# Optimization experiments

Measured on AMD Instinct MI355X. Metric: run time of the kernel, lower is better.

The kernel has to match this reference:

```python
import jax, jax.numpy as jnp
import numpy as np

D_MODEL = 1024
NUM_HEADS = 16
D_K = D_MODEL // NUM_HEADS
LOCAL_WINDOW = 3
STRIDE = 4


def strided_mask(seq_len):
    # position i attends to j iff j <= i and (i-j <= local_window or (i-j) % stride == 0)
    i = jnp.arange(seq_len)[:, None]
    j = jnp.arange(seq_len)[None, :]
    d = i - j
    return (d >= 0) & ((d <= LOCAL_WINDOW) | (d % STRIDE == 0))


def setup_inputs() -> dict:
    key = jax.random.key(0)
    ks = jax.random.split(key, 11)
    B, S, D = 4, 1024, D_MODEL
    s = 1.0 / np.sqrt(D)
    inp = {
        "Q": jax.random.normal(ks[0], (B, S, D), jnp.float32),
        "K": jax.random.normal(ks[1], (B, S, D), jnp.float32),
        "V": jax.random.normal(ks[2], (B, S, D), jnp.float32),
        "Wq": jax.random.normal(ks[3], (D, D), jnp.float32) * s,
        "bq": jnp.zeros((D,), jnp.float32),
        "Wk": jax.random.normal(ks[4], (D, D), jnp.float32) * s,
        "bk": jnp.zeros((D,), jnp.float32),
        "Wv": jax.random.normal(ks[5], (D, D), jnp.float32) * s,
        "bv": jnp.zeros((D,), jnp.float32),
        "Wo": jax.random.normal(ks[6], (D, D), jnp.float32) * s,
        "bo": jnp.zeros((D,), jnp.float32),
    }
    return inp


def reference(Q, K, V, Wq, bq, Wk, bk, Wv, bv, Wo, bo):
    B, S, D = Q.shape
    H, dk = NUM_HEADS, D_K

    def split(x):  # [B,S,D] -> [B,H,S,dk]
        return x.reshape(B, S, H, dk).transpose(0, 2, 1, 3)

    q = split(Q @ Wq + bq)
    k = split(K @ Wk + bk)
    v = split(V @ Wv + bv)

    scores = jnp.einsum("bhsd,bhtd->bhst", q, k) / jnp.sqrt(
        jnp.asarray(dk, jnp.float32))
    m = strided_mask(S)[None, None]  # [1,1,S,S]
    scores = jnp.where(m, scores, -1e9)
    attn = jax.nn.softmax(scores, axis=-1)
    out = jnp.einsum("bhst,bhtd->bhsd", attn, v)
    out = out.transpose(0, 2, 1, 3).reshape(B, S, D)  # combine heads
    return out @ Wo + bo
```

## Files before the change

kernel.cpp:

```cpp
#include <hip/hip_runtime.h>

typedef _Float16 f16;
typedef __attribute__((ext_vector_type(8))) _Float16 f16x8;
typedef __attribute__((ext_vector_type(4))) _Float16 f16x4;
typedef __attribute__((ext_vector_type(4))) float f32x4;

#define MFMA16(a, b, c) __builtin_amdgcn_mfma_f32_16x16x32_f16((a), (b), (c), 0, 0, 0)

__device__ __forceinline__ void gld_lds16(const void* g, void* l) {
  __builtin_amdgcn_global_load_lds(
      (__attribute__((address_space(1))) void*)const_cast<void*>(g),
      (__attribute__((address_space(3))) void*)l, 16, 0, 0);
}

__device__ __forceinline__ f16x8 ld8(const f16* p) { return *(const f16x8*)p; }

__global__ __launch_bounds__(256) void cvt_x_kernel(
    const float* __restrict__ Q, const float* __restrict__ K, const float* __restrict__ V,
    f16* __restrict__ oq, f16* __restrict__ ok, f16* __restrict__ ov) {
  const float* src = blockIdx.z == 0 ? Q : (blockIdx.z == 1 ? K : V);
  f16* dst = blockIdx.z == 0 ? oq : (blockIdx.z == 1 ? ok : ov);
  size_t i = ((size_t)blockIdx.x * 256 + threadIdx.x) * 8;
  float4 a = *(const float4*)(src + i);
  float4 b = *(const float4*)(src + i + 4);
  f16x8 h;
  h[0] = (f16)a.x; h[1] = (f16)a.y; h[2] = (f16)a.z; h[3] = (f16)a.w;
  h[4] = (f16)b.x; h[5] = (f16)b.y; h[6] = (f16)b.z; h[7] = (f16)b.w;
  *(f16x8*)(dst + i) = h;
}

__global__ __launch_bounds__(256) void cvt_wT_kernel(
    const float* __restrict__ Wq, const float* __restrict__ Wk,
    const float* __restrict__ Wv, const float* __restrict__ Wo,
    f16* __restrict__ Tq, f16* __restrict__ Tk, f16* __restrict__ Tv, f16* __restrict__ To) {
  const int z = blockIdx.z;
  const float* W = z == 0 ? Wq : (z == 1 ? Wk : (z == 2 ? Wv : Wo));
  f16* T = z == 0 ? Tq : (z == 1 ? Tk : (z == 2 ? Tv : To));
  __shared__ float tile[64][65];
  const int k0 = blockIdx.x * 64, n0 = blockIdx.y * 64;
  const int tx = threadIdx.x & 63, ty = threadIdx.x >> 6;
#pragma unroll
  for (int rr = 0; rr < 16; ++rr) {
    int r = rr * 4 + ty;
    tile[r][tx] = W[(size_t)(k0 + r) * 1024 + n0 + tx];
  }
  __syncthreads();
#pragma unroll
  for (int rr = 0; rr < 16; ++rr) {
    int nn = rr * 4 + ty;
    T[(size_t)(n0 + nn) * 1024 + k0 + tx] = (f16)tile[tx][nn];
  }
}

__global__ __launch_bounds__(256) void gemm_qkv_kernel(
    const f16* __restrict__ Xq, const f16* __restrict__ Xk, const f16* __restrict__ Xv,
    const f16* __restrict__ Bq, const f16* __restrict__ Bk, const f16* __restrict__ Bv,
    const float* __restrict__ bq, const float* __restrict__ bk, const float* __restrict__ bv,
    f16* __restrict__ qh, f16* __restrict__ kg,
    f16* __restrict__ vh, f16* __restrict__ vtg) {
  const int z = blockIdx.z;
  const f16* A = z == 0 ? Xq : (z == 1 ? Xk : Xv);
  const f16* Bt = z == 0 ? Bq : (z == 1 ? Bk : Bv);
  const float* bias = z == 0 ? bq : (z == 1 ? bk : bv);

  __shared__ alignas(16) f16 lA[128 * 32];
  __shared__ alignas(16) f16 lB[64 * 32];

  const int t = threadIdx.x;
  const int w = t >> 6, lane = t & 63, quad = lane >> 4, l15 = lane & 15;
  const int wm = w >> 1, wn = w & 1;
  const int mbase = blockIdx.x * 128;
  const int nbase = blockIdx.y * 64;

  const f32x4 zero4 = {0.f, 0.f, 0.f, 0.f};
  f32x4 acc[4][2];
#pragma unroll
  for (int mi = 0; mi < 4; ++mi)
#pragma unroll
    for (int ni = 0; ni < 2; ++ni) acc[mi][ni] = zero4;

  const int r = t >> 2;
  const int koff = (t & 3) * 8;

  for (int k0 = 0; k0 < 1024; k0 += 32) {
    __syncthreads();
    gld_lds16(A + (size_t)(mbase + r) * 1024 + k0 + koff, (char*)lA + w * 1024);
    gld_lds16(A + (size_t)(mbase + 64 + r) * 1024 + k0 + koff, (char*)lA + 4096 + w * 1024);
    gld_lds16(Bt + (size_t)(nbase + r) * 1024 + k0 + koff, (char*)lB + w * 1024);
    __syncthreads();

    f16x8 af[4], bf[2];
#pragma unroll
    for (int mi = 0; mi < 4; ++mi)
      af[mi] = ld8(&lA[(wm * 64 + mi * 16 + l15) * 32 + quad * 8]);
#pragma unroll
    for (int ni = 0; ni < 2; ++ni)
      bf[ni] = ld8(&lB[(wn * 32 + ni * 16 + l15) * 32 + quad * 8]);
#pragma unroll
    for (int mi = 0; mi < 4; ++mi)
#pragma unroll
      for (int ni = 0; ni < 2; ++ni)
        acc[mi][ni] = MFMA16(af[mi], bf[ni], acc[mi][ni]);
  }

#pragma unroll
  for (int mi = 0; mi < 4; ++mi) {
#pragma unroll
    for (int ni = 0; ni < 2; ++ni) {
#pragma unroll
      for (int rg = 0; rg < 4; ++rg) {
        const int row = mbase + wm * 64 + mi * 16 + quad * 4 + rg;
        const int col = nbase + wn * 32 + ni * 16 + l15;
        const float v = acc[mi][ni][rg] + bias[col];
        const int bh = (row >> 10) * 16 + (col >> 6);
        const int s = row & 1023, d = col & 63;
        const f16 hv = (f16)v;
        if (z == 0) {
          qh[(size_t)bh * 65536 + s * 64 + d] = hv;
        } else if (z == 1) {
          kg[(((size_t)bh * 4 + (s & 3)) * 256 + (s >> 2)) * 64 + d] = hv;
        } else {
          vh[(size_t)bh * 65536 + s * 64 + d] = hv;
          const int rr = s & 3, n = s >> 2, wi = n & 63;
          vtg[(size_t)bh * 65536 + (size_t)rr * 16384 + (size_t)d * 256 +
              (n & ~63) + ((wi & 15) << 2) + (wi >> 4)] = hv;
        }
      }
    }
  }
}

__global__ __launch_bounds__(256) void gemm_out_kernel(
    const f16* __restrict__ A, const f16* __restrict__ Bt,
    const float* __restrict__ bias, float* __restrict__ Cf) {
  __shared__ alignas(16) f16 lA[64 * 32];
  __shared__ alignas(16) f16 lB[64 * 32];

  const int t = threadIdx.x;
  const int w = t >> 6, lane = t & 63, quad = lane >> 4, l15 = lane & 15;
  const int wm = w >> 1, wn = w & 1;
  const int mbase = blockIdx.x * 64;
  const int nbase = blockIdx.y * 64;

  const f32x4 zero4 = {0.f, 0.f, 0.f, 0.f};
  f32x4 acc[2][2];
#pragma unroll
  for (int mi = 0; mi < 2; ++mi)
#pragma unroll
    for (int ni = 0; ni < 2; ++ni) acc[mi][ni] = zero4;

  const int r = t >> 2;
  const int koff = (t & 3) * 8;

  for (int k0 = 0; k0 < 1024; k0 += 32) {
    __syncthreads();
    gld_lds16(A + (size_t)(mbase + r) * 1024 + k0 + koff, (char*)lA + w * 1024);
    gld_lds16(Bt + (size_t)(nbase + r) * 1024 + k0 + koff, (char*)lB + w * 1024);
    __syncthreads();

    f16x8 af[2], bf[2];
#pragma unroll
    for (int mi = 0; mi < 2; ++mi)
      af[mi] = ld8(&lA[(wm * 32 + mi * 16 + l15) * 32 + quad * 8]);
#pragma unroll
    for (int ni = 0; ni < 2; ++ni)
      bf[ni] = ld8(&lB[(wn * 32 + ni * 16 + l15) * 32 + quad * 8]);
#pragma unroll
    for (int mi = 0; mi < 2; ++mi)
#pragma unroll
      for (int ni = 0; ni < 2; ++ni)
        acc[mi][ni] = MFMA16(af[mi], bf[ni], acc[mi][ni]);
  }

#pragma unroll
  for (int mi = 0; mi < 2; ++mi)
#pragma unroll
    for (int ni = 0; ni < 2; ++ni)
#pragma unroll
      for (int rg = 0; rg < 4; ++rg) {
        const int row = mbase + wm * 32 + mi * 16 + quad * 4 + rg;
        const int col = nbase + wn * 32 + ni * 16 + l15;
        Cf[(size_t)row * 1024 + col] = acc[mi][ni][rg] + bias[col];
      }
}

__global__ __launch_bounds__(256) void attn_far_kernel(
    const f16* __restrict__ qh, const f16* __restrict__ kg,
    const f16* __restrict__ vtg, float* __restrict__ po, float* __restrict__ ml) {
  const int t = threadIdx.x;
  const int w = t >> 6, lane = t & 63, quad = lane >> 4, l15 = lane & 15;
  const int widx = blockIdx.x + 512 * w;
  const int bh = (widx & 255) >> 2, r = widx & 3;
  const int wq = widx >> 8;
  const int m0 = wq * 32;
  const int ntiles = (wq >> 1) + 1;

  __shared__ alignas(16) f16 lp[4][2][16 * 72];

  const f16* qb = qh + (size_t)bh * 65536;
  const f16* kb = kg + ((size_t)bh * 4 + r) * 16384;
  const f16* vb = vtg + (size_t)bh * 65536 + (size_t)r * 16384;
  const float SCL2 = 0.125f * 1.44269504f;

  f16x8 aq[2][2];
#pragma unroll
  for (int mt = 0; mt < 2; ++mt) {
    const int i = 4 * (m0 + mt * 16 + l15) + r;
#pragma unroll
    for (int ko = 0; ko < 2; ++ko)
      aq[mt][ko] = ld8(qb + (size_t)i * 64 + ko * 32 + quad * 8);
  }

  const f32x4 zero4 = {0.f, 0.f, 0.f, 0.f};
  f32x4 o[2][4];
  float mrun[2][4], lrun[2][4];
#pragma unroll
  for (int mt = 0; mt < 2; ++mt)
#pragma unroll
    for (int i = 0; i < 4; ++i) {
      o[mt][i] = zero4; mrun[mt][i] = -1e30f; lrun[mt][i] = 0.f;
    }

  for (int jt = 0; jt < ntiles; ++jt) {
    const int n0 = jt * 64;
    f16x8 bk0[4], bk1[4], bv0[4], bv1[4];
#pragma unroll
    for (int nt = 0; nt < 4; ++nt) {
      const f16* kr = kb + (size_t)(n0 + nt * 16 + l15) * 64;
      bk0[nt] = ld8(kr + quad * 8);
      bk1[nt] = ld8(kr + 32 + quad * 8);
      const f16* vr = vb + (size_t)(nt * 16 + l15) * 256 + n0;
      bv0[nt] = ld8(vr + quad * 8);
      bv1[nt] = ld8(vr + 32 + quad * 8);
    }
    const bool lastt = (jt == ntiles - 1);
#pragma unroll
    for (int mt = 0; mt < 2; ++mt) {
      f32x4 sc[4];
#pragma unroll
      for (int nt = 0; nt < 4; ++nt) {
        f32x4 c = MFMA16(aq[mt][0], bk0[nt], zero4);
        sc[nt] = MFMA16(aq[mt][1], bk1[nt], c);
      }
#pragma unroll
      for (int rg = 0; rg < 4; ++rg) {
        const int m = m0 + mt * 16 + quad * 4 + rg;
        float s[4];
#pragma unroll
        for (int nt = 0; nt < 4; ++nt) {
          float vsc = sc[nt][rg] * SCL2;
          if (lastt) vsc = (n0 + nt * 16 + l15 < m) ? vsc : -3.0e38f;
          s[nt] = vsc;
        }
        float tm = fmaxf(fmaxf(s[0], s[1]), fmaxf(s[2], s[3]));
        tm = fmaxf(tm, __shfl_xor(tm, 1));
        tm = fmaxf(tm, __shfl_xor(tm, 2));
        tm = fmaxf(tm, __shfl_xor(tm, 4));
        tm = fmaxf(tm, __shfl_xor(tm, 8));
        const float mnew = fmaxf(mrun[mt][rg], tm);
        const float alpha = exp2f(mrun[mt][rg] - mnew);
        float p[4], ps = 0.f;
#pragma unroll
        for (int nt = 0; nt < 4; ++nt) { p[nt] = exp2f(s[nt] - mnew); ps += p[nt]; }
        ps += __shfl_xor(ps, 1);
        ps += __shfl_xor(ps, 2);
        ps += __shfl_xor(ps, 4);
        ps += __shfl_xor(ps, 8);
        lrun[mt][rg] = lrun[mt][rg] * alpha + ps;
        mrun[mt][rg] = mnew;
#pragma unroll
        for (int ntv = 0; ntv < 4; ++ntv) o[mt][ntv][rg] *= alpha;
        f16x4 pk;
        pk.x = (f16)p[0]; pk.y = (f16)p[1]; pk.z = (f16)p[2]; pk.w = (f16)p[3];
        *(f16x4*)&lp[w][mt][(quad * 4 + rg) * 72 + l15 * 4] = pk;
      }
    }
#pragma unroll
    for (int mt = 0; mt < 2; ++mt) {
      const f16x8 ap0 = ld8(&lp[w][mt][l15 * 72 + quad * 8]);
      const f16x8 ap1 = ld8(&lp[w][mt][l15 * 72 + 32 + quad * 8]);
#pragma unroll
      for (int ntv = 0; ntv < 4; ++ntv) {
        f32x4 c = MFMA16(ap0, bv0[ntv], o[mt][ntv]);
        o[mt][ntv] = MFMA16(ap1, bv1[ntv], c);
      }
    }
  }

#pragma unroll
  for (int mt = 0; mt < 2; ++mt)
#pragma unroll
    for (int rg = 0; rg < 4; ++rg) {
      const int i = 4 * (m0 + mt * 16 + quad * 4 + rg) + r;
      const size_t idx = (size_t)bh * 1024 + i;
#pragma unroll
      for (int ntv = 0; ntv < 4; ++ntv)
        po[idx * 64 + ntv * 16 + l15] = o[mt][ntv][rg];
      if (l15 == 0) { ml[idx * 2] = mrun[mt][rg]; ml[idx * 2 + 1] = lrun[mt][rg]; }
    }
}

__global__ __launch_bounds__(256) void attn_diag_kernel(
    const f16* __restrict__ qh, const f16* __restrict__ kg, const f16* __restrict__ vh,
    const float* __restrict__ po, const float* __restrict__ ml, f16* __restrict__ ao) {
  const int t = threadIdx.x;
  const int widx = blockIdx.x * 4 + (t >> 6);
  const int l = t & 63;
  const int bh = widx >> 10, i = widx & 1023;
  const float SCL2 = 0.125f * 1.44269504f;

  const float q = (float)qh[(size_t)bh * 65536 + (size_t)i * 64 + l];
  float s[4];
#pragma unroll
  for (int d = 0; d < 4; ++d) {
    const int j = i - d;
    const int jc = j < 0 ? 0 : j;
    float pr = q * (float)kg[(((size_t)bh * 4 + (jc & 3)) * 256 + (jc >> 2)) * 64 + l];
    pr += __shfl_xor(pr, 1);
    pr += __shfl_xor(pr, 2);
    pr += __shfl_xor(pr, 4);
    pr += __shfl_xor(pr, 8);
    pr += __shfl_xor(pr, 16);
    pr += __shfl_xor(pr, 32);
    s[d] = (j >= 0) ? pr * SCL2 : -3.0e38f;
  }
  const float md = fmaxf(fmaxf(s[0], s[1]), fmaxf(s[2], s[3]));
  const size_t idx = (size_t)bh * 1024 + i;
  const float mf = ml[idx * 2], lf = ml[idx * 2 + 1];
  const float M = fmaxf(md, mf);
  float p[4], ld = 0.f;
#pragma unroll
  for (int d = 0; d < 4; ++d) { p[d] = exp2f(s[d] - M); ld += p[d]; }
  float ov = 0.f;
#pragma unroll
  for (int d = 0; d < 4; ++d) {
    const int jc = (i - d) < 0 ? 0 : (i - d);
    ov += p[d] * (float)vh[(size_t)bh * 65536 + (size_t)jc * 64 + l];
  }
  const float fs = exp2f(mf - M);
  const float lt = lf * fs + ld;
  const float of = po[idx * 64 + l];
  const float res = (of * fs + ov) / lt;
  const int b = bh >> 4, h = bh & 15;
  ao[((size_t)(b * 1024 + i)) * 1024 + h * 64 + l] = (f16)res;
}

extern "C" void kernel_launch(void* const* d_in, const int* in_sizes, int n_in,
                              void* d_out, int out_size, void* d_ws, size_t ws_size,
                              hipStream_t stream) {
  const float* Q = (const float*)d_in[0];
  const float* K = (const float*)d_in[1];
  const float* V = (const float*)d_in[2];
  const float* Wq = (const float*)d_in[3];
  const float* bq = (const float*)d_in[4];
  const float* Wk = (const float*)d_in[5];
  const float* bk = (const float*)d_in[6];
  const float* Wv = (const float*)d_in[7];
  const float* bv = (const float*)d_in[8];
  const float* Wo = (const float*)d_in[9];
  const float* bo = (const float*)d_in[10];
  float* out = (float*)d_out;

  char* ws = (char*)d_ws;
  const size_t MB = 1ull << 20;
  f16* TWo = (f16*)(ws + 0 * MB);
  f16* TWq = (f16*)(ws + 2 * MB);
  f16* TWk = (f16*)(ws + 4 * MB);
  f16* TWv = (f16*)(ws + 6 * MB);
  f16* Xq  = (f16*)(ws + 8 * MB);
  f16* Xk  = (f16*)(ws + 16 * MB);
  f16* Xv  = (f16*)(ws + 24 * MB);
  f16* qhb = (f16*)(ws + 32 * MB);
  f16* vhb = (f16*)(ws + 40 * MB);
  f16* kgb = (f16*)(ws + 48 * MB);
  f16* vtg = (f16*)(ws + 56 * MB);
  float* po  = (float*)(ws + 8 * MB);
  float* mlb = (float*)(ws + 24 * MB);
  f16* aob   = (f16*)(ws + 56 * MB);

  cvt_x_kernel<<<dim3(2048, 1, 3), 256, 0, stream>>>(Q, K, V, Xq, Xk, Xv);
  cvt_wT_kernel<<<dim3(16, 16, 4), 256, 0, stream>>>(Wq, Wk, Wv, Wo, TWq, TWk, TWv, TWo);
  gemm_qkv_kernel<<<dim3(32, 16, 3), 256, 0, stream>>>(
      Xq, Xk, Xv, TWq, TWk, TWv, bq, bk, bv, qhb, kgb, vhb, vtg);
  attn_far_kernel<<<dim3(512), 256, 0, stream>>>(qhb, kgb, vtg, po, mlb);
  attn_diag_kernel<<<dim3(16384), 256, 0, stream>>>(qhb, kgb, vhb, po, mlb, aob);
  gemm_out_kernel<<<dim3(64, 16), 256, 0, stream>>>(aob, TWo, bo, out);
}
```

Measured before the change: 232.8 us.

## Merge conversion kernels, widen GEMM N tiles, shrink attention wave tiles

Fuses the activation cast and weight transpose kernels into one prep launch. Doubles the N tile of both GEMMs to 128 so each wave issues more MFMAs per LDS fragment load, halving the grid. Halves the per-wave query tile in the far-attention kernel to 16 rows and doubles the grid, trading reuse of K/V loads for more parallel waves and fewer registers. The changes target launch overhead, GEMM operand reuse and attention occupancy/load balance respectively.

```diff
diff --git a/kernel.cpp b/kernel.cpp
--- a/kernel.cpp
+++ b/kernel.cpp
@@ -15,40 +15,43 @@
 
 __device__ __forceinline__ f16x8 ld8(const f16* p) { return *(const f16x8*)p; }
 
-__global__ __launch_bounds__(256) void cvt_x_kernel(
+__global__ __launch_bounds__(256) void prep_kernel(
     const float* __restrict__ Q, const float* __restrict__ K, const float* __restrict__ V,
-    f16* __restrict__ oq, f16* __restrict__ ok, f16* __restrict__ ov) {
-  const float* src = blockIdx.z == 0 ? Q : (blockIdx.z == 1 ? K : V);
-  f16* dst = blockIdx.z == 0 ? oq : (blockIdx.z == 1 ? ok : ov);
-  size_t i = ((size_t)blockIdx.x * 256 + threadIdx.x) * 8;
-  float4 a = *(const float4*)(src + i);
-  float4 b = *(const float4*)(src + i + 4);
-  f16x8 h;
-  h[0] = (f16)a.x; h[1] = (f16)a.y; h[2] = (f16)a.z; h[3] = (f16)a.w;
-  h[4] = (f16)b.x; h[5] = (f16)b.y; h[6] = (f16)b.z; h[7] = (f16)b.w;
-  *(f16x8*)(dst + i) = h;
-}
-
-__global__ __launch_bounds__(256) void cvt_wT_kernel(
     const float* __restrict__ Wq, const float* __restrict__ Wk,
     const float* __restrict__ Wv, const float* __restrict__ Wo,
+    f16* __restrict__ Xq, f16* __restrict__ Xk, f16* __restrict__ Xv,
     f16* __restrict__ Tq, f16* __restrict__ Tk, f16* __restrict__ Tv, f16* __restrict__ To) {
-  const int z = blockIdx.z;
-  const float* W = z == 0 ? Wq : (z == 1 ? Wk : (z == 2 ? Wv : Wo));
-  f16* T = z == 0 ? Tq : (z == 1 ? Tk : (z == 2 ? Tv : To));
+  const int bx = blockIdx.x;
   __shared__ float tile[64][65];
-  const int k0 = blockIdx.x * 64, n0 = blockIdx.y * 64;
-  const int tx = threadIdx.x & 63, ty = threadIdx.x >> 6;
-#pragma unroll
-  for (int rr = 0; rr < 16; ++rr) {
-    int r = rr * 4 + ty;
-    tile[r][tx] = W[(size_t)(k0 + r) * 1024 + n0 + tx];
-  }
-  __syncthreads();
-#pragma unroll
-  for (int rr = 0; rr < 16; ++rr) {
-    int nn = rr * 4 + ty;
-    T[(size_t)(n0 + nn) * 1024 + k0 + tx] = (f16)tile[tx][nn];
+  if (bx < 6144) {
+    const int z = bx >> 11, blk = bx & 2047;
+    const float* src = z == 0 ? Q : (z == 1 ? K : V);
+    f16* dst = z == 0 ? Xq : (z == 1 ? Xk : Xv);
+    size_t i = ((size_t)blk * 256 + threadIdx.x) * 8;
+    float4 a = *(const float4*)(src + i);
+    float4 b = *(const float4*)(src + i + 4);
+    f16x8 h;
+    h[0] = (f16)a.x; h[1] = (f16)a.y; h[2] = (f16)a.z; h[3] = (f16)a.w;
+    h[4] = (f16)b.x; h[5] = (f16)b.y; h[6] = (f16)b.z; h[7] = (f16)b.w;
+    *(f16x8*)(dst + i) = h;
+  } else {
+    const int idx = bx - 6144;
+    const int z = idx >> 8, xy = idx & 255;
+    const float* W = z == 0 ? Wq : (z == 1 ? Wk : (z == 2 ? Wv : Wo));
+    f16* T = z == 0 ? Tq : (z == 1 ? Tk : (z == 2 ? Tv : To));
+    const int k0 = (xy & 15) * 64, n0 = (xy >> 4) * 64;
+    const int tx = threadIdx.x & 63, ty = threadIdx.x >> 6;
+#pragma unroll
+    for (int rr = 0; rr < 16; ++rr) {
+      int r = rr * 4 + ty;
+      tile[r][tx] = W[(size_t)(k0 + r) * 1024 + n0 + tx];
+    }
+    __syncthreads();
+#pragma unroll
+    for (int rr = 0; rr < 16; ++rr) {
+      int nn = rr * 4 + ty;
+      T[(size_t)(n0 + nn) * 1024 + k0 + tx] = (f16)tile[tx][nn];
+    }
   }
 }
 
@@ -64,20 +67,20 @@
   const float* bias = z == 0 ? bq : (z == 1 ? bk : bv);
 
   __shared__ alignas(16) f16 lA[128 * 32];
-  __shared__ alignas(16) f16 lB[64 * 32];
+  __shared__ alignas(16) f16 lB[128 * 32];
 
   const int t = threadIdx.x;
   const int w = t >> 6, lane = t & 63, quad = lane >> 4, l15 = lane & 15;
   const int wm = w >> 1, wn = w & 1;
   const int mbase = blockIdx.x * 128;
-  const int nbase = blockIdx.y * 64;
+  const int nbase = blockIdx.y * 128;
 
   const f32x4 zero4 = {0.f, 0.f, 0.f, 0.f};
-  f32x4 acc[4][2];
+  f32x4 acc[4][4];
 #pragma unroll
   for (int mi = 0; mi < 4; ++mi)
 #pragma unroll
-    for (int ni = 0; ni < 2; ++ni) acc[mi][ni] = zero4;
+    for (int ni = 0; ni < 4; ++ni) acc[mi][ni] = zero4;
 
   const int r = t >> 2;
   const int koff = (t & 3) * 8;
@@ -87,30 +90,31 @@
     gld_lds16(A + (size_t)(mbase + r) * 1024 + k0 + koff, (char*)lA + w * 1024);
     gld_lds16(A + (size_t)(mbase + 64 + r) * 1024 + k0 + koff, (char*)lA + 4096 + w * 1024);
     gld_lds16(Bt + (size_t)(nbase + r) * 1024 + k0 + koff, (char*)lB + w * 1024);
-    __syncthreads();
-
-    f16x8 af[4], bf[2];
+    gld_lds16(Bt + (size_t)(nbase + 64 + r) * 1024 + k0 + koff, (char*)lB + 4096 + w * 1024);
+    __syncthreads();
+
+    f16x8 af[4], bf[4];
 #pragma unroll
     for (int mi = 0; mi < 4; ++mi)
       af[mi] = ld8(&lA[(wm * 64 + mi * 16 + l15) * 32 + quad * 8]);
 #pragma unroll
-    for (int ni = 0; ni < 2; ++ni)
-      bf[ni] = ld8(&lB[(wn * 32 + ni * 16 + l15) * 32 + quad * 8]);
+    for (int ni = 0; ni < 4; ++ni)
+      bf[ni] = ld8(&lB[(wn * 64 + ni * 16 + l15) * 32 + quad * 8]);
 #pragma unroll
     for (int mi = 0; mi < 4; ++mi)
 #pragma unroll
-      for (int ni = 0; ni < 2; ++ni)
+      for (int ni = 0; ni < 4; ++ni)
         acc[mi][ni] = MFMA16(af[mi], bf[ni], acc[mi][ni]);
   }
 
 #pragma unroll
   for (int mi = 0; mi < 4; ++mi) {
 #pragma unroll
-    for (int ni = 0; ni < 2; ++ni) {
+    for (int ni = 0; ni < 4; ++ni) {
 #pragma unroll
       for (int rg = 0; rg < 4; ++rg) {
         const int row = mbase + wm * 64 + mi * 16 + quad * 4 + rg;
-        const int col = nbase + wn * 32 + ni * 16 + l15;
+        const int col = nbase + wn * 64 + ni * 16 + l15;
         const float v = acc[mi][ni][rg] + bias[col];
         const int bh = (row >> 10) * 16 + (col >> 6);
         const int s = row & 1023, d = col & 63;
@@ -134,20 +138,20 @@
     const f16* __restrict__ A, const f16* __restrict__ Bt,
     const float* __restrict__ bias, float* __restrict__ Cf) {
   __shared__ alignas(16) f16 lA[64 * 32];
-  __shared__ alignas(16) f16 lB[64 * 32];
+  __shared__ alignas(16) f16 lB[128 * 32];
 
   const int t = threadIdx.x;
   const int w = t >> 6, lane = t & 63, quad = lane >> 4, l15 = lane & 15;
   const int wm = w >> 1, wn = w & 1;
   const int mbase = blockIdx.x * 64;
-  const int nbase = blockIdx.y * 64;
+  const int nbase = blockIdx.y * 128;
 
   const f32x4 zero4 = {0.f, 0.f, 0.f, 0.f};
-  f32x4 acc[2][2];
+  f32x4 acc[2][4];
 #pragma unroll
   for (int mi = 0; mi < 2; ++mi)
 #pragma unroll
-    for (int ni = 0; ni < 2; ++ni) acc[mi][ni] = zero4;
+    for (int ni = 0; ni < 4; ++ni) acc[mi][ni] = zero4;
 
   const int r = t >> 2;
   const int koff = (t & 3) * 8;
@@ -156,30 +160,31 @@
     __syncthreads();
     gld_lds16(A + (size_t)(mbase + r) * 1024 + k0 + koff, (char*)lA + w * 1024);
     gld_lds16(Bt + (size_t)(nbase + r) * 1024 + k0 + koff, (char*)lB + w * 1024);
-    __syncthreads();
-
-    f16x8 af[2], bf[2];
+    gld_lds16(Bt + (size_t)(nbase + 64 + r) * 1024 + k0 + koff, (char*)lB + 4096 + w * 1024);
+    __syncthreads();
+
+    f16x8 af[2], bf[4];
 #pragma unroll
     for (int mi = 0; mi < 2; ++mi)
       af[mi] = ld8(&lA[(wm * 32 + mi * 16 + l15) * 32 + quad * 8]);
 #pragma unroll
-    for (int ni = 0; ni < 2; ++ni)
-      bf[ni] = ld8(&lB[(wn * 32 + ni * 16 + l15) * 32 + quad * 8]);
+    for (int ni = 0; ni < 4; ++ni)
+      bf[ni] = ld8(&lB[(wn * 64 + ni * 16 + l15) * 32 + quad * 8]);
 #pragma unroll
     for (int mi = 0; mi < 2; ++mi)
 #pragma unroll
-      for (int ni = 0; ni < 2; ++ni)
+      for (int ni = 0; ni < 4; ++ni)
         acc[mi][ni] = MFMA16(af[mi], bf[ni], acc[mi][ni]);
   }
 
 #pragma unroll
   for (int mi = 0; mi < 2; ++mi)
 #pragma unroll
-    for (int ni = 0; ni < 2; ++ni)
+    for (int ni = 0; ni < 4; ++ni)
 #pragma unroll
       for (int rg = 0; rg < 4; ++rg) {
         const int row = mbase + wm * 32 + mi * 16 + quad * 4 + rg;
-        const int col = nbase + wn * 32 + ni * 16 + l15;
+        const int col = nbase + wn * 64 + ni * 16 + l15;
         Cf[(size_t)row * 1024 + col] = acc[mi][ni][rg] + bias[col];
       }
 }
@@ -189,37 +194,28 @@
     const f16* __restrict__ vtg, float* __restrict__ po, float* __restrict__ ml) {
   const int t = threadIdx.x;
   const int w = t >> 6, lane = t & 63, quad = lane >> 4, l15 = lane & 15;
-  const int widx = blockIdx.x + 512 * w;
+  const int widx = blockIdx.x + 1024 * w;
   const int bh = (widx & 255) >> 2, r = widx & 3;
   const int wq = widx >> 8;
-  const int m0 = wq * 32;
-  const int ntiles = (wq >> 1) + 1;
-
-  __shared__ alignas(16) f16 lp[4][2][16 * 72];
+  const int m0 = wq * 16;
+  const int ntiles = (wq >> 2) + 1;
+
+  __shared__ alignas(16) f16 lp[4][16 * 72];
 
   const f16* qb = qh + (size_t)bh * 65536;
   const f16* kb = kg + ((size_t)bh * 4 + r) * 16384;
   const f16* vb = vtg + (size_t)bh * 65536 + (size_t)r * 16384;
   const float SCL2 = 0.125f * 1.44269504f;
 
-  f16x8 aq[2][2];
-#pragma unroll
-  for (int mt = 0; mt < 2; ++mt) {
-    const int i = 4 * (m0 + mt * 16 + l15) + r;
-#pragma unroll
-    for (int ko = 0; ko < 2; ++ko)
-      aq[mt][ko] = ld8(qb + (size_t)i * 64 + ko * 32 + quad * 8);
-  }
+  const f16* qrow = qb + (size_t)(4 * (m0 + l15) + r) * 64;
+  const f16x8 aq0 = ld8(qrow + quad * 8);
+  const f16x8 aq1 = ld8(qrow + 32 + quad * 8);
 
   const f32x4 zero4 = {0.f, 0.f, 0.f, 0.f};
-  f32x4 o[2][4];
-  float mrun[2][4], lrun[2][4];
-#pragma unroll
-  for (int mt = 0; mt < 2; ++mt)
-#pragma unroll
-    for (int i = 0; i < 4; ++i) {
-      o[mt][i] = zero4; mrun[mt][i] = -1e30f; lrun[mt][i] = 0.f;
-    }
+  f32x4 o[4];
+  float mrun[4], lrun[4];
+#pragma unroll
+  for (int i = 0; i < 4; ++i) { o[i] = zero4; mrun[i] = -1e30f; lrun[i] = 0.f; }
 
   for (int jt = 0; jt < ntiles; ++jt) {
     const int n0 = jt * 64;
@@ -233,71 +229,63 @@
       bv0[nt] = ld8(vr + quad * 8);
       bv1[nt] = ld8(vr + 32 + quad * 8);
     }
+    f32x4 sc[4];
+#pragma unroll
+    for (int nt = 0; nt < 4; ++nt) {
+      f32x4 c = MFMA16(aq0, bk0[nt], zero4);
+      sc[nt] = MFMA16(aq1, bk1[nt], c);
+    }
     const bool lastt = (jt == ntiles - 1);
 #pragma unroll
-    for (int mt = 0; mt < 2; ++mt) {
-      f32x4 sc[4];
+    for (int rg = 0; rg < 4; ++rg) {
+      const int m = m0 + quad * 4 + rg;
+      float s[4];
 #pragma unroll
       for (int nt = 0; nt < 4; ++nt) {
-        f32x4 c = MFMA16(aq[mt][0], bk0[nt], zero4);
-        sc[nt] = MFMA16(aq[mt][1], bk1[nt], c);
+        float vsc = sc[nt][rg] * SCL2;
+        if (lastt) vsc = (n0 + nt * 16 + l15 < m) ? vsc : -3.0e38f;
+        s[nt] = vsc;
       }
-#pragma unroll
-      for (int rg = 0; rg < 4; ++rg) {
-        const int m = m0 + mt * 16 + quad * 4 + rg;
-        float s[4];
-#pragma unroll
-        for (int nt = 0; nt < 4; ++nt) {
-          float vsc = sc[nt][rg] * SCL2;
-          if (lastt) vsc = (n0 + nt * 16 + l15 < m) ? vsc : -3.0e38f;
-          s[nt] = vsc;
-        }
-        float tm = fmaxf(fmaxf(s[0], s[1]), fmaxf(s[2], s[3]));
-        tm = fmaxf(tm, __shfl_xor(tm, 1));
-        tm = fmaxf(tm, __shfl_xor(tm, 2));
-        tm = fmaxf(tm, __shfl_xor(tm, 4));
-        tm = fmaxf(tm, __shfl_xor(tm, 8));
-        const float mnew = fmaxf(mrun[mt][rg], tm);
-        const float alpha = exp2f(mrun[mt][rg] - mnew);
-        float p[4], ps = 0.f;
-#pragma unroll
-        for (int nt = 0; nt < 4; ++nt) { p[nt] = exp2f(s[nt] - mnew); ps += p[nt]; }
-        ps += __shfl_xor(ps, 1);
-        ps += __shfl_xor(ps, 2);
-        ps += __shfl_xor(ps, 4);
-        ps += __shfl_xor(ps, 8);
-        lrun[mt][rg] = lrun[mt][rg] * alpha + ps;
-        mrun[mt][rg] = mnew;
-#pragma unroll
-        for (int ntv = 0; ntv < 4; ++ntv) o[mt][ntv][rg] *= alpha;
-        f16x4 pk;
-        pk.x = (f16)p[0]; pk.y = (f16)p[1]; pk.z = (f16)p[2]; pk.w = (f16)p[3];
-        *(f16x4*)&lp[w][mt][(quad * 4 + rg) * 72 + l15 * 4] = pk;
-      }
-    }
-#pragma unroll
-    for (int mt = 0; mt < 2; ++mt) {
-      const f16x8 ap0 = ld8(&lp[w][mt][l15 * 72 + quad * 8]);
-      const f16x8 ap1 = ld8(&lp[w][mt][l15 * 72 + 32 + quad * 8]);
-#pragma unroll
-      for (int ntv = 0; ntv < 4; ++ntv) {
-        f32x4 c = MFMA16(ap0, bv0[ntv], o[mt][ntv]);
-        o[mt][ntv] = MFMA16(ap1, bv1[ntv], c);
-      }
-    }
-  }
-
-#pragma unroll
-  for (int mt = 0; mt < 2; ++mt)
-#pragma unroll
-    for (int rg = 0; rg < 4; ++rg) {
-      const int i = 4 * (m0 + mt * 16 + quad * 4 + rg) + r;
-      const size_t idx = (size_t)bh * 1024 + i;
-#pragma unroll
-      for (int ntv = 0; ntv < 4; ++ntv)
-        po[idx * 64 + ntv * 16 + l15] = o[mt][ntv][rg];
-      if (l15 == 0) { ml[idx * 2] = mrun[mt][rg]; ml[idx * 2 + 1] = lrun[mt][rg]; }
-    }
+      float tm = fmaxf(fmaxf(s[0], s[1]), fmaxf(s[2], s[3]));
+      tm = fmaxf(tm, __shfl_xor(tm, 1));
+      tm = fmaxf(tm, __shfl_xor(tm, 2));
+      tm = fmaxf(tm, __shfl_xor(tm, 4));
+      tm = fmaxf(tm, __shfl_xor(tm, 8));
+      const float mnew = fmaxf(mrun[rg], tm);
+      const float alpha = exp2f(mrun[rg] - mnew);
+      float p[4], ps = 0.f;
+#pragma unroll
+      for (int nt = 0; nt < 4; ++nt) { p[nt] = exp2f(s[nt] - mnew); ps += p[nt]; }
+      ps += __shfl_xor(ps, 1);
+      ps += __shfl_xor(ps, 2);
+      ps += __shfl_xor(ps, 4);
+      ps += __shfl_xor(ps, 8);
+      lrun[rg] = lrun[rg] * alpha + ps;
+      mrun[rg] = mnew;
+#pragma unroll
+      for (int ntv = 0; ntv < 4; ++ntv) o[ntv][rg] *= alpha;
+      f16x4 pk;
+      pk.x = (f16)p[0]; pk.y = (f16)p[1]; pk.z = (f16)p[2]; pk.w = (f16)p[3];
+      *(f16x4*)&lp[w][(quad * 4 + rg) * 72 + l15 * 4] = pk;
+    }
+    const f16x8 ap0 = ld8(&lp[w][l15 * 72 + quad * 8]);
+    const f16x8 ap1 = ld8(&lp[w][l15 * 72 + 32 + quad * 8]);
+#pragma unroll
+    for (int ntv = 0; ntv < 4; ++ntv) {
+      f32x4 c = MFMA16(ap0, bv0[ntv], o[ntv]);
+      o[ntv] = MFMA16(ap1, bv1[ntv], c);
+    }
+  }
+
+#pragma unroll
+  for (int rg = 0; rg < 4; ++rg) {
+    const int i = 4 * (m0 + quad * 4 + rg) + r;
+    const size_t idx = (size_t)bh * 1024 + i;
+#pragma unroll
+    for (int ntv = 0; ntv < 4; ++ntv)
+      po[idx * 64 + ntv * 16 + l15] = o[ntv][rg];
+    if (l15 == 0) { ml[idx * 2] = mrun[rg]; ml[idx * 2 + 1] = lrun[rg]; }
+  }
 }
 
 __global__ __launch_bounds__(256) void attn_diag_kernel(
@@ -378,11 +366,11 @@
   float* mlb = (float*)(ws + 24 * MB);
   f16* aob   = (f16*)(ws + 56 * MB);
 
-  cvt_x_kernel<<<dim3(2048, 1, 3), 256, 0, stream>>>(Q, K, V, Xq, Xk, Xv);
-  cvt_wT_kernel<<<dim3(16, 16, 4), 256, 0, stream>>>(Wq, Wk, Wv, Wo, TWq, TWk, TWv, TWo);
-  gemm_qkv_kernel<<<dim3(32, 16, 3), 256, 0, stream>>>(
+  prep_kernel<<<dim3(7168), 256, 0, stream>>>(
+      Q, K, V, Wq, Wk, Wv, Wo, Xq, Xk, Xv, TWq, TWk, TWv, TWo);
+  gemm_qkv_kernel<<<dim3(32, 8, 3), 256, 0, stream>>>(
       Xq, Xk, Xv, TWq, TWk, TWv, bq, bk, bv, qhb, kgb, vhb, vtg);
-  attn_far_kernel<<<dim3(512), 256, 0, stream>>>(qhb, kgb, vtg, po, mlb);
+  attn_far_kernel<<<dim3(1024), 256, 0, stream>>>(qhb, kgb, vtg, po, mlb);
   attn_diag_kernel<<<dim3(16384), 256, 0, stream>>>(qhb, kgb, vhb, po, mlb, aob);
-  gemm_out_kernel<<<dim3(64, 16), 256, 0, stream>>>(aob, TWo, bo, out);
-}
+  gemm_out_kernel<<<dim3(64, 8), 256, 0, stream>>>(aob, TWo, bo, out);
+}
```

New measurement: 238.9 us. 2.6% more time.
